# Optimization experiments

Hardware: AMD Instinct MI355X
Metric: run time of the kernel (lower is better)

The kernel has to match this reference:

```python
import jax, jax.numpy as jnp
import numpy as np

G = 16          # spline grid_size
NT = 32         # num_tiles
NS = 2          # num_states
SD = 8          # state_dim
MAXLEN = 2048.0 # max_seq_len
SPREAD = 2.0    # position_spread
LN_EPS = 1e-5


def cubic_bspline(t):
    t = jnp.abs(t)
    r1 = 2.0 / 3.0 - t * t + 0.5 * t ** 3
    r2 = (1.0 / 6.0) * (2.0 - t) ** 3
    return jnp.where(t < 1.0, r1, jnp.where(t < 2.0, r2, jnp.zeros_like(t)))


def ternary(x):
    return jnp.where(x > 0.3, 1.0, jnp.where(x < -0.3, -1.0, 0.0)).astype(x.dtype)


def setup_inputs() -> dict:
    key = jax.random.key(0)
    ks = jax.random.split(key, 14)
    B, T, D = 4, 2048, 1024
    H = D // 4
    x = jax.random.normal(ks[0], (B, T, D), jnp.float32)
    positions = jnp.broadcast_to(jnp.arange(T, dtype=jnp.float32), (B, T))
    states = jax.random.randint(ks[1], (B, T), 0, NS)
    ln_gamma = jnp.ones((D,), jnp.float32)
    ln_beta = jnp.zeros((D,), jnp.float32)
    W1 = jax.random.normal(ks[2], (D, H), jnp.float32) * (1.0 / np.sqrt(D))
    b1 = jnp.zeros((H,), jnp.float32)
    W2 = jax.random.normal(ks[3], (H, 2), jnp.float32) * (1.0 / np.sqrt(H))
    b2 = jnp.zeros((2,), jnp.float32)
    spline_coeffs = jax.random.normal(ks[4], (NT, G, G, 3), jnp.float32) * 0.5
    spline_scales = jnp.ones((NT,), jnp.float32)
    directions = jax.random.normal(ks[5], (NT, D), jnp.float32) * 0.02
    state_signatures = jax.random.normal(ks[6], (NT, SD), jnp.float32) * 0.1
    state_emb = jax.random.normal(ks[7], (NS, SD), jnp.float32)
    state_mod = jnp.ones((NS, NT), jnp.float32)
    output_scale = jnp.ones((1,), jnp.float32) * 0.1
    return dict(x=x, positions=positions, states=states, ln_gamma=ln_gamma,
                ln_beta=ln_beta, W1=W1, b1=b1, W2=W2, b2=b2,
                spline_coeffs=spline_coeffs, spline_scales=spline_scales,
                directions=directions, state_signatures=state_signatures,
                state_emb=state_emb, state_mod=state_mod, output_scale=output_scale)


def reference(x, positions, states, ln_gamma, ln_beta, W1, b1, W2, b2,
              spline_coeffs, spline_scales, directions, state_signatures,
              state_emb, state_mod, output_scale):
    B, T, D = x.shape
    xf = x.reshape(-1, D)                               # [N, D]
    mu = jnp.mean(xf, axis=-1, keepdims=True)
    var = jnp.mean((xf - mu) ** 2, axis=-1, keepdims=True)
    xn = (xf - mu) / jnp.sqrt(var + LN_EPS) * ln_gamma + ln_beta

    # --- three-way routing ---
    sigs = jnp.sign(directions)                         # ternary signatures [NT, D]
    content = xn @ sigs.T                               # [N, NT]
    pos = positions.reshape(-1)
    pn = pos / MAXLEN * NT
    centers = jnp.arange(NT, dtype=xn.dtype)
    spatial = cubic_bspline((pn[:, None] - centers[None, :]) / SPREAD)  # [N, NT]
    st = states.reshape(-1)
    sv = state_emb[st]                                  # [N, SD]
    temporal = jax.nn.sigmoid(sv @ state_signatures.T)  # [N, NT]
    combined = content * spatial * temporal
    probs = jax.nn.softmax(combined * 5.0, axis=-1)
    tile_idx = jnp.argmax(combined, axis=-1)            # [N]
    tile_weights = jnp.take_along_axis(probs, tile_idx[:, None], axis=1)[:, 0]

    # --- compress to 2D spline coordinates ---
    h = jax.nn.gelu(xn @ W1 + b1, approximate=False)
    comp = jnp.tanh(h @ W2 + b2)                        # [N, 2]
    a, b = comp[:, 0], comp[:, 1]

    # --- ternary 2D spline per winning tile (vectorized dispatch) ---
    idx_a = jnp.clip(((a + 1.0) / 2.0 * G).astype(jnp.int32), 0, G - 1)
    idx_b = jnp.clip(((b + 1.0) / 2.0 * G).astype(jnp.int32), 0, G - 1)
    q = spline_coeffs + jax.lax.stop_gradient(ternary(spline_coeffs) - spline_coeffs)
    cell = q[tile_idx, idx_a, idx_b]                    # [N, 3]
    cs = 2.0 / G
    la = (a + 1.0 - idx_a.astype(a.dtype) * cs) / cs
    lb = (b + 1.0 - idx_b.astype(b.dtype) * cs) / cs
    scale = (cell[:, 0] + cell[:, 1] * la + cell[:, 2] * lb) * spline_scales[tile_idx]
    smod = state_mod[st, tile_idx]
    contrib = (scale * smod)[:, None] * directions[tile_idx]  # [N, D]

    out = x + contrib.reshape(B, T, D) * output_scale   # residual, eval (no dropout)
    return out
```

## Files before the change

### kernel.cpp

```cpp
#include <hip/hip_runtime.h>
#include <math.h>

#define NROWS 8192
#define DD    1024
#define HH    256
#define NTT   32
#define NCOLS 288
#define BM    32
#define BK    64
#define NW    12
#define HPS   292

typedef __attribute__((ext_vector_type(8))) __bf16 bf16x8;
typedef __attribute__((ext_vector_type(4))) float f32x4;
typedef __attribute__((ext_vector_type(8))) unsigned short ushort8_t;

static __device__ __forceinline__ unsigned short f2bf(float f) {
    unsigned int u = __float_as_uint(f);
    unsigned int r = (u + 0x7fffu + ((u >> 16) & 1u)) >> 16;
    return (unsigned short)r;
}

static __device__ __forceinline__ float bf2f(unsigned short u) {
    return __uint_as_float(((unsigned int)u) << 16);
}

static __device__ __forceinline__ float sgnf(float x) {
    return x > 0.0f ? 1.0f : (x < 0.0f ? -1.0f : 0.0f);
}

static __device__ __forceinline__ float ternf(float x) {
    return x > 0.3f ? 1.0f : (x < -0.3f ? -1.0f : 0.0f);
}

static __device__ __forceinline__ float bspline(float u) {
    float t = fabsf(u);
    if (t < 1.0f) return 0.66666666666666663f - t * t + 0.5f * t * t * t;
    if (t < 2.0f) { float w = 2.0f - t; return 0.16666666666666666f * w * w * w; }
    return 0.0f;
}

__global__ __launch_bounds__(256) void k_prep(const float* __restrict__ W1,
                                              const float* __restrict__ dirs,
                                              const float* __restrict__ gamma,
                                              const float* __restrict__ beta,
                                              unsigned short* __restrict__ WT,
                                              float* __restrict__ colsum,
                                              float* __restrict__ bwv) {
    int bid = blockIdx.x;
    int tid = threadIdx.x;
    if (bid < 256) {
        __shared__ float tile[32][33];
        __shared__ float redg[8][32];
        __shared__ float redb[8][32];
        int ktile = bid & 31;
        int ntile = bid >> 5;
        int tx = tid & 31;
        int ty = tid >> 5;
        float sg = 0.f, sb = 0.f;
#pragma unroll
        for (int i = 0; i < 4; ++i) {
            int k = ktile * 32 + ty + i * 8;
            int n = ntile * 32 + tx;
            float w = W1[(size_t)k * HH + n];
            float gk = gamma[k];
            tile[ty + i * 8][tx] = w * gk;
            sg += w * gk;
            sb += w * beta[k];
        }
        redg[ty][tx] = sg;
        redb[ty][tx] = sb;
        __syncthreads();
#pragma unroll
        for (int i = 0; i < 4; ++i) {
            int n = ntile * 32 + ty + i * 8;
            int k = ktile * 32 + tx;
            WT[(size_t)n * DD + k] = f2bf(tile[tx][ty + i * 8]);
        }
        if (ty == 0) {
            float a = 0.f, c = 0.f;
#pragma unroll
            for (int k = 0; k < 8; ++k) { a += redg[k][tx]; c += redb[k][tx]; }
            int j = ntile * 32 + tx;
            atomicAdd(&colsum[j], a);
            atomicAdd(&bwv[j], c);
        }
    } else {
        int r = bid - 256;
        float4 v  = ((const float4*)(dirs + (size_t)r * DD))[tid];
        float4 g  = ((const float4*)gamma)[tid];
        float4 be = ((const float4*)beta)[tid];
        float s0 = sgnf(v.x), s1 = sgnf(v.y), s2 = sgnf(v.z), s3 = sgnf(v.w);
        ushort4 o;
        o.x = f2bf(s0 * g.x); o.y = f2bf(s1 * g.y);
        o.z = f2bf(s2 * g.z); o.w = f2bf(s3 * g.w);
        ((ushort4*)(WT + (size_t)(HH + r) * DD))[tid] = o;
        float ps = s0 * g.x + s1 * g.y + s2 * g.z + s3 * g.w;
        float pb = s0 * be.x + s1 * be.y + s2 * be.z + s3 * be.w;
#pragma unroll
        for (int off = 32; off; off >>= 1) {
            ps += __shfl_xor(ps, off);
            pb += __shfl_xor(pb, off);
        }
        __shared__ float red[8];
        int wid = tid >> 6, lane = tid & 63;
        if (lane == 0) { red[wid] = ps; red[wid + 4] = pb; }
        __syncthreads();
        if (tid == 0) {
            colsum[HH + r] = red[0] + red[1] + red[2] + red[3];
            bwv[HH + r]    = red[4] + red[5] + red[6] + red[7];
        }
    }
}

__global__ __launch_bounds__(768, 3) void k_fused(
    const float* __restrict__ x, const unsigned short* __restrict__ WT,
    const float* __restrict__ colsum, const float* __restrict__ bwv,
    const float* __restrict__ positions, const int* __restrict__ states,
    const float* __restrict__ b1, const float* __restrict__ W2,
    const float* __restrict__ b2, const float* __restrict__ spc,
    const float* __restrict__ sps, const float* __restrict__ dirs,
    const float* __restrict__ ssig, const float* __restrict__ semb,
    const float* __restrict__ smod, const float* __restrict__ oscale,
    float* __restrict__ out) {
    __shared__ short Xl[BM * DD];
    __shared__ short Bl[2][NCOLS * BK];
    __shared__ float stats[BM][2];
    float* HPl = (float*)&Bl[0][0];

    int tid  = threadIdx.x;
    int row0 = blockIdx.x * BM;
    int lane = tid & 63;
    int wid  = tid >> 6;
    int wn = wid % 6, wm = wid / 6;
    int l15 = lane & 15, l4 = lane >> 4;

    int rA = tid >> 3;
    int g8 = tid & 7;
    const float* xrow = x + (size_t)(row0 + rA) * DD + g8 * 8;
    int xbase = rA * 2048 + ((g8 * 16) ^ ((rA & 7) << 4));

    float s = 0.f, sq = 0.f;
    float4 x0a, x0b, x1a, x1b;
    f32x4 acc[3];
#pragma unroll
    for (int nf = 0; nf < 3; ++nf) acc[nf] = (f32x4){0.f, 0.f, 0.f, 0.f};

#define STAGE_B(kt, buf)                                                         \
    {                                                                            \
        _Pragma("unroll")                                                        \
        for (int ci = 0; ci < 3; ++ci) {                                         \
            int li = ci * 768 + tid;                                             \
            int r  = li >> 3;                                                    \
            int g  = li & 7;                                                     \
            const unsigned short* src =                                          \
                WT + (size_t)r * DD + (kt) * 64 + ((g * 8) ^ ((r & 7) << 3));    \
            __builtin_amdgcn_global_load_lds(                                    \
                (const __attribute__((address_space(1))) void*)(const void*)src, \
                (__attribute__((address_space(3))) void*)(void*)(Bl[buf] + li * 8), \
                16, 0, 0);                                                       \
        }                                                                        \
    }

#define WRITE_A(XA, XB, KT)                                                     \
    if (wid < 4) {                                                              \
        s  += (XA.x + XA.y + XA.z + XA.w) + (XB.x + XB.y + XB.z + XB.w);        \
        sq += (XA.x*XA.x + XA.y*XA.y + XA.z*XA.z + XA.w*XA.w)                   \
            + (XB.x*XB.x + XB.y*XB.y + XB.z*XB.z + XB.w*XB.w);                  \
        ushort8_t w;                                                            \
        w[0] = f2bf(XA.x); w[1] = f2bf(XA.y); w[2] = f2bf(XA.z); w[3] = f2bf(XA.w); \
        w[4] = f2bf(XB.x); w[5] = f2bf(XB.y); w[6] = f2bf(XB.z); w[7] = f2bf(XB.w); \
        *(ushort8_t*)((char*)Xl + xbase + (KT) * 128) = w;                      \
    }

#define COMPUTE(KT, CUR)                                                        \
    _Pragma("unroll")                                                           \
    for (int ks = 0; ks < 2; ++ks) {                                            \
        int ra = wm * 16 + l15;                                                 \
        int ca = (KT) * 128 + ((ks * 64 + l4 * 16) ^ ((ra & 7) << 4));          \
        bf16x8 av = *(const bf16x8*)((const char*)Xl + ra * 2048 + ca);         \
        bf16x8 bv[3];                                                           \
        _Pragma("unroll")                                                       \
        for (int nf = 0; nf < 3; ++nf) {                                        \
            int rb = wn * 48 + nf * 16 + l15;                                   \
            int cb = (ks * 64 + l4 * 16) ^ ((rb & 7) << 4);                     \
            bv[nf] = *(const bf16x8*)((const char*)Bl[CUR] + rb * 128 + cb);    \
        }                                                                       \
        _Pragma("unroll")                                                       \
        for (int nf = 0; nf < 3; ++nf)                                          \
            acc[nf] = __builtin_amdgcn_mfma_f32_16x16x32_bf16(av, bv[nf], acc[nf], 0, 0, 0); \
    }

#define STEP(kt, XCa, XCb, XIa, XIb, CUR, NXT)                                  \
    {                                                                           \
        if ((kt) <= 14) STAGE_B((kt) + 1, NXT);                                 \
        __builtin_amdgcn_sched_barrier(0);                                      \
        if ((kt) <= 13 && wid < 4) {                                            \
            XIa = ((const float4*)(xrow + ((kt) + 2) * 64))[0];                 \
            XIb = ((const float4*)(xrow + ((kt) + 2) * 64))[1];                 \
        }                                                                       \
        COMPUTE(kt, CUR);                                                       \
        if ((kt) <= 14) WRITE_A(XCa, XCb, (kt) + 1);                            \
        if ((kt) <= 13) {                                                       \
            if (wid < 4) asm volatile("s_waitcnt vmcnt(2) lgkmcnt(0)" ::: "memory"); \
            else         asm volatile("s_waitcnt vmcnt(0)" ::: "memory");       \
        } else if ((kt) == 14) {                                                \
            if (wid < 4) asm volatile("s_waitcnt vmcnt(0) lgkmcnt(0)" ::: "memory"); \
            else         asm volatile("s_waitcnt vmcnt(0)" ::: "memory");       \
        }                                                                       \
        if ((kt) <= 14) {                                                       \
            __builtin_amdgcn_s_barrier();                                       \
            __builtin_amdgcn_sched_barrier(0);                                  \
        }                                                                       \
    }

    STAGE_B(0, 0);
    __builtin_amdgcn_sched_barrier(0);
    if (wid < 4) {
        x0a = ((const float4*)(xrow))[0];
        x0b = ((const float4*)(xrow))[1];
        x1a = ((const float4*)(xrow + 64))[0];
        x1b = ((const float4*)(xrow + 64))[1];
    }
    WRITE_A(x0a, x0b, 0);
    if (wid < 4) asm volatile("s_waitcnt vmcnt(2) lgkmcnt(0)" ::: "memory");
    else         asm volatile("s_waitcnt vmcnt(0)" ::: "memory");
    __builtin_amdgcn_s_barrier();
    __builtin_amdgcn_sched_barrier(0);

    for (int kt = 0; kt < 16; kt += 2) {
        STEP(kt,     x1a, x1b, x0a, x0b, 0, 1);
        STEP(kt + 1, x0a, x0b, x1a, x1b, 1, 0);
    }
    __syncthreads();

    if (wid < 4) {
        s  += __shfl_xor(s, 1);  s  += __shfl_xor(s, 2);  s  += __shfl_xor(s, 4);
        sq += __shfl_xor(sq, 1); sq += __shfl_xor(sq, 2); sq += __shfl_xor(sq, 4);
        if (g8 == 0) {
            float mu  = s * (1.0f / DD);
            float var = sq * (1.0f / DD) - mu * mu;
            stats[rA][0] = mu;
            stats[rA][1] = rsqrtf(var + 1e-5f);
        }
    }
    __syncthreads();

#pragma unroll
    for (int nf = 0; nf < 3; ++nf) {
        int colg = wn * 48 + nf * 16 + l15;
        float cs = colsum[colg];
        float bw = bwv[colg];
        int r0 = wm * 16 + l4 * 4;
#pragma unroll
        for (int i = 0; i < 4; ++i) {
            float mu = stats[r0 + i][0], rs = stats[r0 + i][1];
            HPl[(r0 + i) * HPS + colg] = rs * acc[nf][i] - mu * rs * cs + bw;
        }
    }
    __syncthreads();

    float4 b1v = ((const float4*)b1)[lane];
    float w2a[4], w2b[4];
#pragma unroll
    for (int i = 0; i < 4; ++i) {
        int j = lane * 4 + i;
        w2a[i] = W2[2 * j];
        w2b[i] = W2[2 * j + 1];
    }
    float tvs[2] = {0.f, 0.f};
    if (lane < NTT) {
#pragma unroll
        for (int s2 = 0; s2 < 2; ++s2) {
            float d0 = 0.f;
#pragma unroll
            for (int k = 0; k < 8; ++k) d0 += semb[s2 * 8 + k] * ssig[lane * 8 + k];
            tvs[s2] = 1.0f / (1.0f + expf(-d0));
        }
    }
    float osc = oscale[0];
    float bb0 = b2[0], bb1 = b2[1];

    for (int r = wid; r < BM; r += NW) {
        int row = row0 + r;
        float4 hv = *(const float4*)&HPl[r * HPS + lane * 4];
        float hs[4] = {hv.x, hv.y, hv.z, hv.w};
        float bs[4] = {b1v.x, b1v.y, b1v.z, b1v.w};
        float sa = 0.f, sb2 = 0.f;
#pragma unroll
        for (int i = 0; i < 4; ++i) {
            float h = hs[i] + bs[i];
            float g = 0.5f * h * (1.0f + erff(h * 0.70710678118654752f));
            sa  += g * w2a[i];
            sb2 += g * w2b[i];
        }
#pragma unroll
        for (int off = 32; off; off >>= 1) {
            sa  += __shfl_xor(sa, off);
            sb2 += __shfl_xor(sb2, off);
        }
        float av2 = tanhf(sa + bb0);
        float bv2 = tanhf(sb2 + bb1);

        int st = states[row];
        float comb;
        if (lane < NTT) {
            float content = HPl[r * HPS + HH + lane];
            float pn = positions[row] * ((float)NTT / 2048.0f);
            float spv = bspline((pn - (float)lane) * 0.5f);
            comb = content * spv * tvs[st];
        } else {
            comb = -__builtin_inff();
        }
        int bi = lane;
#pragma unroll
        for (int off = 32; off; off >>= 1) {
            float ov = __shfl_xor(comb, off);
            int   oi = __shfl_xor(bi, off);
            if (ov > comb || (ov == comb && oi < bi)) { comb = ov; bi = oi; }
        }
        int ia = (int)((av2 + 1.0f) * 8.0f); ia = ia < 0 ? 0 : (ia > 15 ? 15 : ia);
        int ib = (int)((bv2 + 1.0f) * 8.0f); ib = ib < 0 ? 0 : (ib > 15 ? 15 : ib);
        const float* cc = spc + (((size_t)bi * 16 + ia) * 16 + ib) * 3;
        float c0 = ternf(cc[0]), c1 = ternf(cc[1]), c2 = ternf(cc[2]);
        float la = (av2 + 1.0f - (float)ia * 0.125f) * 8.0f;
        float lb = (bv2 + 1.0f - (float)ib * 0.125f) * 8.0f;
        float scale = (c0 + c1 * la + c2 * lb) * sps[bi];
        float cr = scale * smod[st * NTT + bi] * osc;

        int swzr = (r & 7) << 4;
        const float4* dr = (const float4*)(dirs + (size_t)bi * DD);
        float4* orow = (float4*)(out + (size_t)row * DD);
#pragma unroll
        for (int i = 0; i < 4; ++i) {
            int idx = i * 64 + lane;
            int byteoff = r * 2048 + ((idx * 8) ^ swzr);
            ushort4 xv = *(const ushort4*)((const char*)Xl + byteoff);
            float4 dv = dr[idx];
            float4 o;
            o.x = fmaf(cr, dv.x, bf2f(xv.x));
            o.y = fmaf(cr, dv.y, bf2f(xv.y));
            o.z = fmaf(cr, dv.z, bf2f(xv.z));
            o.w = fmaf(cr, dv.w, bf2f(xv.w));
            orow[idx] = o;
        }
    }
#undef STAGE_B
#undef WRITE_A
#undef COMPUTE
#undef STEP
}

extern "C" void kernel_launch(void* const* d_in, const int* in_sizes, int n_in,
                              void* d_out, int out_size, void* d_ws, size_t ws_size,
                              hipStream_t stream) {
    const float* x     = (const float*)d_in[0];
    const float* pos   = (const float*)d_in[1];
    const int*   st    = (const int*)d_in[2];
    const float* gam   = (const float*)d_in[3];
    const float* bet   = (const float*)d_in[4];
    const float* W1    = (const float*)d_in[5];
    const float* b1    = (const float*)d_in[6];
    const float* W2    = (const float*)d_in[7];
    const float* b2    = (const float*)d_in[8];
    const float* spc   = (const float*)d_in[9];
    const float* sps   = (const float*)d_in[10];
    const float* dirs  = (const float*)d_in[11];
    const float* ssig  = (const float*)d_in[12];
    const float* semb  = (const float*)d_in[13];
    const float* smod  = (const float*)d_in[14];
    const float* oscal = (const float*)d_in[15];
    float* out = (float*)d_out;

    char* ws = (char*)d_ws;
    unsigned short* WT = (unsigned short*)ws;
    float* colsum = (float*)(ws + 589824);
    float* bwv    = (float*)(ws + 589824 + 288 * 4);

    hipMemsetAsync(colsum, 0, 2 * 288 * sizeof(float), stream);
    k_prep<<<288, 256, 0, stream>>>(W1, dirs, gam, bet, WT, colsum, bwv);
    k_fused<<<NROWS / BM, 768, 0, stream>>>(x, WT, colsum, bwv, pos, st, b1, W2, b2,
                                            spc, sps, dirs, ssig, semb, smod, oscal, out);
}
```

Baseline: 41.32 us.

## Regrid fused GEMM to 9 waves with 2x2 MFMA tiles and drop atomics/memset

The fused kernel moves from 12 waves (2x6 grid, 16x48 per wave) to 9 waves, each owning all 32 rows and 32 columns. Each wave now issues a 2x2 set of MFMA tiles, so every loaded B fragment is reused across two A fragments. The prep kernel writes per-k-tile partial column sums instead of using atomics, which removes the memset launch. The fused kernel reduces those partials into shared memory at startup. This trades one launch and the atomic contention for extra partial-sum reads in every block. Launch bounds go to 576 threads with min 1 block, which changes register and occupancy limits, and the remaining waves of the x-staging path must still line up with the new thread mapping.

```diff
diff --git a/kernel.cpp b/kernel.cpp
--- a/kernel.cpp
+++ b/kernel.cpp
@@ -8,7 +8,8 @@
 #define NCOLS 288
 #define BM    32
 #define BK    64
-#define NW    12
+#define NTHR  576
+#define NW    9
 #define HPS   292
 
 typedef __attribute__((ext_vector_type(8))) __bf16 bf16x8;
@@ -45,8 +46,8 @@
                                               const float* __restrict__ gamma,
                                               const float* __restrict__ beta,
                                               unsigned short* __restrict__ WT,
-                                              float* __restrict__ colsum,
-                                              float* __restrict__ bwv) {
+                                              float* __restrict__ colsumP,
+                                              float* __restrict__ bwP) {
     int bid = blockIdx.x;
     int tid = threadIdx.x;
     if (bid < 256) {
@@ -82,8 +83,8 @@
 #pragma unroll
             for (int k = 0; k < 8; ++k) { a += redg[k][tx]; c += redb[k][tx]; }
             int j = ntile * 32 + tx;
-            atomicAdd(&colsum[j], a);
-            atomicAdd(&bwv[j], c);
+            colsumP[ktile * NCOLS + j] = a;
+            bwP[ktile * NCOLS + j]     = c;
         }
     } else {
         int r = bid - 256;
@@ -105,17 +106,21 @@
         __shared__ float red[8];
         int wid = tid >> 6, lane = tid & 63;
         if (lane == 0) { red[wid] = ps; red[wid + 4] = pb; }
+        if (tid < 31) {
+            colsumP[(tid + 1) * NCOLS + HH + r] = 0.f;
+            bwP[(tid + 1) * NCOLS + HH + r]     = 0.f;
+        }
         __syncthreads();
         if (tid == 0) {
-            colsum[HH + r] = red[0] + red[1] + red[2] + red[3];
-            bwv[HH + r]    = red[4] + red[5] + red[6] + red[7];
-        }
-    }
-}
-
-__global__ __launch_bounds__(768, 3) void k_fused(
+            colsumP[HH + r] = red[0] + red[1] + red[2] + red[3];
+            bwP[HH + r]     = red[4] + red[5] + red[6] + red[7];
+        }
+    }
+}
+
+__global__ __launch_bounds__(NTHR, 1) void k_fused(
     const float* __restrict__ x, const unsigned short* __restrict__ WT,
-    const float* __restrict__ colsum, const float* __restrict__ bwv,
+    const float* __restrict__ colsumP, const float* __restrict__ bwP,
     const float* __restrict__ positions, const int* __restrict__ states,
     const float* __restrict__ b1, const float* __restrict__ W2,
     const float* __restrict__ b2, const float* __restrict__ spc,
@@ -126,31 +131,49 @@
     __shared__ short Xl[BM * DD];
     __shared__ short Bl[2][NCOLS * BK];
     __shared__ float stats[BM][2];
+    __shared__ float Csum_l[NCOLS];
+    __shared__ float Bw_l[NCOLS];
     float* HPl = (float*)&Bl[0][0];
 
     int tid  = threadIdx.x;
     int row0 = blockIdx.x * BM;
     int lane = tid & 63;
     int wid  = tid >> 6;
-    int wn = wid % 6, wm = wid / 6;
+    int wn = wid;
     int l15 = lane & 15, l4 = lane >> 4;
+
+    if (tid < NCOLS) {
+        float a = 0.f;
+#pragma unroll 8
+        for (int k = 0; k < 32; ++k) a += colsumP[k * NCOLS + tid];
+        Csum_l[tid] = a;
+    } else if (tid < 2 * NCOLS) {
+        int j = tid - NCOLS;
+        float c = 0.f;
+#pragma unroll 8
+        for (int k = 0; k < 32; ++k) c += bwP[k * NCOLS + j];
+        Bw_l[j] = c;
+    }
+    __builtin_amdgcn_sched_barrier(0);
 
     int rA = tid >> 3;
     int g8 = tid & 7;
-    const float* xrow = x + (size_t)(row0 + rA) * DD + g8 * 8;
-    int xbase = rA * 2048 + ((g8 * 16) ^ ((rA & 7) << 4));
+    const float* xrow = x + (size_t)(row0 + (rA & 31)) * DD + g8 * 8;
+    int xbase = (rA & 31) * 2048 + ((g8 * 16) ^ ((rA & 7) << 4));
 
     float s = 0.f, sq = 0.f;
     float4 x0a, x0b, x1a, x1b;
-    f32x4 acc[3];
-#pragma unroll
-    for (int nf = 0; nf < 3; ++nf) acc[nf] = (f32x4){0.f, 0.f, 0.f, 0.f};
+    f32x4 acc[2][2];
+#pragma unroll
+    for (int i = 0; i < 2; ++i)
+#pragma unroll
+        for (int j = 0; j < 2; ++j) acc[i][j] = (f32x4){0.f, 0.f, 0.f, 0.f};
 
 #define STAGE_B(kt, buf)                                                         \
     {                                                                            \
         _Pragma("unroll")                                                        \
-        for (int ci = 0; ci < 3; ++ci) {                                         \
-            int li = ci * 768 + tid;                                             \
+        for (int ci = 0; ci < 4; ++ci) {                                         \
+            int li = ci * NTHR + tid;                                            \
             int r  = li >> 3;                                                    \
             int g  = li & 7;                                                     \
             const unsigned short* src =                                          \
@@ -176,19 +199,25 @@
 #define COMPUTE(KT, CUR)                                                        \
     _Pragma("unroll")                                                           \
     for (int ks = 0; ks < 2; ++ks) {                                            \
-        int ra = wm * 16 + l15;                                                 \
-        int ca = (KT) * 128 + ((ks * 64 + l4 * 16) ^ ((ra & 7) << 4));          \
-        bf16x8 av = *(const bf16x8*)((const char*)Xl + ra * 2048 + ca);         \
-        bf16x8 bv[3];                                                           \
+        bf16x8 av[2], bv[2];                                                    \
         _Pragma("unroll")                                                       \
-        for (int nf = 0; nf < 3; ++nf) {                                        \
-            int rb = wn * 48 + nf * 16 + l15;                                   \
+        for (int mf = 0; mf < 2; ++mf) {                                        \
+            int ra = mf * 16 + l15;                                             \
+            int ca = (KT) * 128 + ((ks * 64 + l4 * 16) ^ ((ra & 7) << 4));      \
+            av[mf] = *(const bf16x8*)((const char*)Xl + ra * 2048 + ca);        \
+        }                                                                       \
+        _Pragma("unroll")                                                       \
+        for (int nf = 0; nf < 2; ++nf) {                                        \
+            int rb = wn * 32 + nf * 16 + l15;                                   \
             int cb = (ks * 64 + l4 * 16) ^ ((rb & 7) << 4);                     \
             bv[nf] = *(const bf16x8*)((const char*)Bl[CUR] + rb * 128 + cb);    \
         }                                                                       \
         _Pragma("unroll")                                                       \
-        for (int nf = 0; nf < 3; ++nf)                                          \
-            acc[nf] = __builtin_amdgcn_mfma_f32_16x16x32_bf16(av, bv[nf], acc[nf], 0, 0, 0); \
+        for (int mf = 0; mf < 2; ++mf)                                          \
+            _Pragma("unroll")                                                   \
+            for (int nf = 0; nf < 2; ++nf)                                      \
+                acc[mf][nf] = __builtin_amdgcn_mfma_f32_16x16x32_bf16(          \
+                    av[mf], bv[nf], acc[mf][nf], 0, 0, 0);                      \
     }
 
 #define STEP(kt, XCa, XCb, XIa, XIb, CUR, NXT)                                  \
@@ -247,15 +276,18 @@
     __syncthreads();
 
 #pragma unroll
-    for (int nf = 0; nf < 3; ++nf) {
-        int colg = wn * 48 + nf * 16 + l15;
-        float cs = colsum[colg];
-        float bw = bwv[colg];
-        int r0 = wm * 16 + l4 * 4;
-#pragma unroll
-        for (int i = 0; i < 4; ++i) {
-            float mu = stats[r0 + i][0], rs = stats[r0 + i][1];
-            HPl[(r0 + i) * HPS + colg] = rs * acc[nf][i] - mu * rs * cs + bw;
+    for (int mf = 0; mf < 2; ++mf) {
+#pragma unroll
+        for (int nf = 0; nf < 2; ++nf) {
+            int colg = wn * 32 + nf * 16 + l15;
+            float cs = Csum_l[colg];
+            float bw = Bw_l[colg];
+            int r0 = mf * 16 + l4 * 4;
+#pragma unroll
+            for (int i = 0; i < 4; ++i) {
+                float mu = stats[r0 + i][0], rs = stats[r0 + i][1];
+                HPl[(r0 + i) * HPS + colg] = rs * acc[mf][nf][i] - mu * rs * cs + bw;
+            }
         }
     }
     __syncthreads();
@@ -374,11 +406,10 @@
 
     char* ws = (char*)d_ws;
     unsigned short* WT = (unsigned short*)ws;
-    float* colsum = (float*)(ws + 589824);
-    float* bwv    = (float*)(ws + 589824 + 288 * 4);
-
-    hipMemsetAsync(colsum, 0, 2 * 288 * sizeof(float), stream);
-    k_prep<<<288, 256, 0, stream>>>(W1, dirs, gam, bet, WT, colsum, bwv);
-    k_fused<<<NROWS / BM, 768, 0, stream>>>(x, WT, colsum, bwv, pos, st, b1, W2, b2,
-                                            spc, sps, dirs, ssig, semb, smod, oscal, out);
-}
+    float* colsumP = (float*)(ws + 589824);
+    float* bwP     = (float*)(ws + 589824 + 36864);
+
+    k_prep<<<288, 256, 0, stream>>>(W1, dirs, gam, bet, WT, colsumP, bwP);
+    k_fused<<<NROWS / BM, NTHR, 0, stream>>>(x, WT, colsumP, bwP, pos, st, b1, W2, b2,
+                                             spc, sps, dirs, ssig, semb, smod, oscal, out);
+}
```

Measured after the change: 41.31 us. Within noise of the previous version (-0.0%).
